# Performance work log

Hardware: AMD Instinct MI355X
Metric: run time of the kernel (lower is better)

## Reference

```python
import jax, jax.numpy as jnp
import numpy as np

S, B, SC = 2048, 1024, 256 * 16  # shops, bundles, styles*colors


def setup_inputs() -> dict:
    key = jax.random.key(0)
    k1, k2, k3, k4 = jax.random.split(key, 4)
    return {
        "proba": jax.random.normal(k1, (S * B,), dtype=jnp.float32),
        "cur_inven": jax.random.uniform(k2, (S, SC), dtype=jnp.float32),
        "bun_sc": jax.random.uniform(k3, (B, SC), dtype=jnp.float32),
        "avail_bundle": jax.random.uniform(k4, (B,), dtype=jnp.float32),
        "alloc_bundle": jnp.zeros((B,), dtype=jnp.float32),
    }


def reference(proba, cur_inven, bun_sc, avail_bundle, alloc_bundle):
    # proba[i] with i = shop*B + bundle  ->  [S, B]
    p = proba.reshape(S, B)
    # constraint_multiplier: 0.01 if over-availability (p>0) or over-negative-alloc (p<0)
    over_avail = (avail_bundle[None, :] - p < 0.0) & (p > 0.0)
    over_alloc = (alloc_bundle[None, :] + p < 0.0) & (p < 0.0)
    cm = jnp.where(over_avail | over_alloc, jnp.float32(0.01), jnp.float32(1.0))
    # next_inven[s, sc] = cur[s, sc] + sum_b bun_sc[b, sc] * p[s, b] * cm[s, b]
    next_inven = cur_inven + jnp.einsum('sb,bc->sc', p * cm, bun_sc)
    return next_inven.reshape(1, -1)
```

## Files before the change

kernel.cpp:

```cpp
#include <hip/hip_runtime.h>

#define S_DIM  2048
#define B_DIM  1024
#define SC_DIM 4096

#define BM 128
#define BN 128
#define BK 64

typedef __bf16 bf16x8 __attribute__((ext_vector_type(8)));
typedef float  f32x4  __attribute__((ext_vector_type(4)));
typedef unsigned short u16x4 __attribute__((ext_vector_type(4)));
typedef unsigned short u16x8 __attribute__((ext_vector_type(8)));

__device__ __forceinline__ unsigned short f2bf(float f) {
    unsigned int u = __builtin_bit_cast(unsigned int, f);
    return (unsigned short)((u + 0x7FFFu + ((u >> 16) & 1u)) >> 16);
}

__device__ __forceinline__ void gld_lds16(const void* g, void* l) {
    __builtin_amdgcn_global_load_lds(
        (const __attribute__((address_space(1))) unsigned int*)g,
        (__attribute__((address_space(3))) unsigned int*)l, 16, 0, 0);
}

__global__ __launch_bounds__(256)
void prepack_a(const float* __restrict__ proba,
               const float* __restrict__ avail,
               const float* __restrict__ alloc,
               unsigned short* __restrict__ wsA)
{
    int c = blockIdx.x * 256 + threadIdx.x;
    int n = c >> 7;
    int G = c & 127;
    int k = G * 8;

    f32x4 p0 = *(const f32x4*)&proba[(size_t)n * B_DIM + k];
    f32x4 p1 = *(const f32x4*)&proba[(size_t)n * B_DIM + k + 4];
    f32x4 av0 = *(const f32x4*)&avail[k];
    f32x4 av1 = *(const f32x4*)&avail[k + 4];
    f32x4 al0 = *(const f32x4*)&alloc[k];
    f32x4 al1 = *(const f32x4*)&alloc[k + 4];

    u16x8 w;
    #pragma unroll
    for (int i = 0; i < 4; ++i) {
        float pv = p0[i];
        bool oa = (av0[i] - pv < 0.f) && (pv > 0.f);
        bool ob = (al0[i] + pv < 0.f) && (pv < 0.f);
        w[i] = f2bf(pv * ((oa || ob) ? 0.01f : 1.0f));
    }
    #pragma unroll
    for (int i = 0; i < 4; ++i) {
        float pv = p1[i];
        bool oa = (av1[i] - pv < 0.f) && (pv > 0.f);
        bool ob = (al1[i] + pv < 0.f) && (pv < 0.f);
        w[4 + i] = f2bf(pv * ((oa || ob) ? 0.01f : 1.0f));
    }
    int Gs = (G & ~7) | ((G & 7) ^ (n & 7));
    *(u16x8*)&wsA[(size_t)n * B_DIM + Gs * 8] = w;
}

__global__ __launch_bounds__(256)
void prepack_b(const float* __restrict__ bsc,
               unsigned short* __restrict__ wsB)
{
    __shared__ float lds[64][129];
    const int t = threadIdx.x;
    const int bn0 = blockIdx.x * 128;
    const int k0  = blockIdx.y * 64;

    #pragma unroll
    for (int p = 0; p < 8; ++p) {
        int kl = (t >> 5) + p * 8;
        int cl = (t & 31) * 4;
        f32x4 v = *(const f32x4*)&bsc[(size_t)(k0 + kl) * SC_DIM + bn0 + cl];
        lds[kl][cl]     = v[0];
        lds[kl][cl + 1] = v[1];
        lds[kl][cl + 2] = v[2];
        lds[kl][cl + 3] = v[3];
    }
    __syncthreads();

    #pragma unroll
    for (int p = 0; p < 4; ++p) {
        int g = t & 7;
        int n = (t >> 3) + p * 32;
        u16x8 w;
        #pragma unroll
        for (int i = 0; i < 8; ++i)
            w[i] = f2bf(lds[g * 8 + i][n]);
        int gs = g ^ (n & 7);
        *(u16x8*)&wsB[(size_t)(bn0 + n) * B_DIM + k0 + gs * 8] = w;
    }
}

__global__ __launch_bounds__(256, 2)
void gemm_pk(const unsigned short* __restrict__ wsA,
             const unsigned short* __restrict__ wsB,
             const float* __restrict__ cur,
             float* __restrict__ out)
{
    __shared__ __align__(16) unsigned short sA[BM * BK];
    __shared__ __align__(16) unsigned short sB[BN * BK];

    const int tid  = threadIdx.x;
    const int lane = tid & 63;
    const int wid  = tid >> 6;
    const int wm   = wid >> 1;
    const int wn   = wid & 1;
    const int l16  = lane & 15;
    const int lg   = lane >> 4;

    const int bm0 = blockIdx.y * BM;
    const int bn0 = blockIdx.x * BN;

    f32x4 acc[4][4];
    #pragma unroll
    for (int i = 0; i < 4; ++i)
        #pragma unroll
        for (int j = 0; j < 4; ++j)
            acc[i][j] = {0.f, 0.f, 0.f, 0.f};

    const int cn = tid >> 3;
    const int cg = tid & 7;

    for (int k0 = 0; k0 < B_DIM; k0 += BK) {
        #pragma unroll
        for (int is = 0; is < 4; ++is) {
            int n = cn + is * 32;
            gld_lds16(wsA + (size_t)(bm0 + n) * B_DIM + k0 + cg * 8,
                      &sA[(is * 256 + tid) * 8]);
        }
        #pragma unroll
        for (int is = 0; is < 4; ++is) {
            int n = cn + is * 32;
            gld_lds16(wsB + (size_t)(bn0 + n) * B_DIM + k0 + cg * 8,
                      &sB[(is * 256 + tid) * 8]);
        }
        __syncthreads();

        #pragma unroll
        for (int kk = 0; kk < 2; ++kk) {
            bf16x8 afr[4], bfr[4];
            #pragma unroll
            for (int mf = 0; mf < 4; ++mf) {
                int r = wm * 64 + mf * 16 + l16;
                afr[mf] = *(const bf16x8*)&sA[r * BK + (((kk * 4 + lg) ^ (r & 7)) * 8)];
            }
            #pragma unroll
            for (int nf = 0; nf < 4; ++nf) {
                int r = wn * 64 + nf * 16 + l16;
                bfr[nf] = *(const bf16x8*)&sB[r * BK + (((kk * 4 + lg) ^ (r & 7)) * 8)];
            }
            #pragma unroll
            for (int mf = 0; mf < 4; ++mf)
                #pragma unroll
                for (int nf = 0; nf < 4; ++nf)
                    acc[mf][nf] = __builtin_amdgcn_mfma_f32_16x16x32_bf16(
                        afr[mf], bfr[nf], acc[mf][nf], 0, 0, 0);
        }
        __syncthreads();
    }

    #pragma unroll
    for (int mf = 0; mf < 4; ++mf) {
        #pragma unroll
        for (int j = 0; j < 4; ++j) {
            int row = bm0 + wm * 64 + mf * 16 + lg * 4 + j;
            #pragma unroll
            for (int nf = 0; nf < 4; ++nf) {
                int col = bn0 + wn * 64 + nf * 16 + l16;
                size_t idx = (size_t)row * SC_DIM + col;
                out[idx] = cur[idx] + acc[mf][nf][j];
            }
        }
    }
}

#define LDK 72
__global__ __launch_bounds__(256, 2)
void opt_gemm_fused(const float* __restrict__ proba,
                    const float* __restrict__ cur,
                    const float* __restrict__ bsc,
                    const float* __restrict__ avail,
                    const float* __restrict__ alloc,
                    float* __restrict__ out)
{
    __shared__ __align__(16) unsigned short sA[BM * LDK];
    __shared__ __align__(16) unsigned short sB[BN * LDK];
    const int tid = threadIdx.x;
    const int lane = tid & 63;
    const int wid = tid >> 6;
    const int wm = wid >> 1, wn = wid & 1;
    const int bm0 = blockIdx.y * BM, bn0 = blockIdx.x * BN;
    const int af4 = tid & 15, ar0 = tid >> 4;
    const int bnn = tid & 127, bkh = tid >> 7;
    const int l16 = lane & 15, lg = lane >> 4;

    f32x4 acc[4][4];
    #pragma unroll
    for (int i = 0; i < 4; ++i)
        #pragma unroll
        for (int j = 0; j < 4; ++j) acc[i][j] = {0.f, 0.f, 0.f, 0.f};

    for (int k0 = 0; k0 < B_DIM; k0 += BK) {
        f32x4 av = *(const f32x4*)&avail[k0 + af4 * 4];
        f32x4 al = *(const f32x4*)&alloc[k0 + af4 * 4];
        #pragma unroll
        for (int pass = 0; pass < 8; ++pass) {
            int r = ar0 + pass * 16;
            f32x4 p = *(const f32x4*)&proba[(size_t)(bm0 + r) * B_DIM + k0 + af4 * 4];
            u16x4 w;
            #pragma unroll
            for (int i = 0; i < 4; ++i) {
                float pv = p[i];
                bool oa = (av[i] - pv < 0.f) && (pv > 0.f);
                bool ob = (al[i] + pv < 0.f) && (pv < 0.f);
                w[i] = f2bf(pv * ((oa || ob) ? 0.01f : 1.0f));
            }
            *(u16x4*)&sA[r * LDK + af4 * 4] = w;
        }
        #pragma unroll
        for (int g = 0; g < 4; ++g) {
            u16x8 w;
            #pragma unroll
            for (int i = 0; i < 8; ++i) {
                int kk = bkh * 32 + g * 8 + i;
                w[i] = f2bf(bsc[(size_t)(k0 + kk) * SC_DIM + bn0 + bnn]);
            }
            *(u16x8*)&sB[bnn * LDK + bkh * 32 + g * 8] = w;
        }
        __syncthreads();
        #pragma unroll
        for (int kk = 0; kk < 2; ++kk) {
            bf16x8 afr[4], bfr[4];
            #pragma unroll
            for (int mf = 0; mf < 4; ++mf)
                afr[mf] = *(const bf16x8*)&sA[(wm * 64 + mf * 16 + l16) * LDK + kk * 32 + lg * 8];
            #pragma unroll
            for (int nf = 0; nf < 4; ++nf)
                bfr[nf] = *(const bf16x8*)&sB[(wn * 64 + nf * 16 + l16) * LDK + kk * 32 + lg * 8];
            #pragma unroll
            for (int mf = 0; mf < 4; ++mf)
                #pragma unroll
                for (int nf = 0; nf < 4; ++nf)
                    acc[mf][nf] = __builtin_amdgcn_mfma_f32_16x16x32_bf16(
                        afr[mf], bfr[nf], acc[mf][nf], 0, 0, 0);
        }
        __syncthreads();
    }
    #pragma unroll
    for (int mf = 0; mf < 4; ++mf)
        #pragma unroll
        for (int j = 0; j < 4; ++j) {
            int row = bm0 + wm * 64 + mf * 16 + lg * 4 + j;
            #pragma unroll
            for (int nf = 0; nf < 4; ++nf) {
                int col = bn0 + wn * 64 + nf * 16 + l16;
                size_t idx = (size_t)row * SC_DIM + col;
                out[idx] = cur[idx] + acc[mf][nf][j];
            }
        }
}

extern "C" void kernel_launch(void* const* d_in, const int* in_sizes, int n_in,
                              void* d_out, int out_size, void* d_ws, size_t ws_size,
                              hipStream_t stream) {
    const float* proba = (const float*)d_in[0];
    const float* cur   = (const float*)d_in[1];
    const float* bsc   = (const float*)d_in[2];
    const float* avail = (const float*)d_in[3];
    const float* alloc = (const float*)d_in[4];
    float* out = (float*)d_out;

    const size_t wsA_bytes = (size_t)S_DIM * B_DIM * 2;
    const size_t wsB_bytes = (size_t)SC_DIM * B_DIM * 2;

    if (ws_size >= wsA_bytes + wsB_bytes) {
        unsigned short* wsA = (unsigned short*)d_ws;
        unsigned short* wsB = (unsigned short*)((char*)d_ws + wsA_bytes);

        prepack_a<<<dim3(S_DIM * B_DIM / 8 / 256), 256, 0, stream>>>(proba, avail, alloc, wsA);
        prepack_b<<<dim3(SC_DIM / 128, B_DIM / 64), 256, 0, stream>>>(bsc, wsB);
        gemm_pk<<<dim3(SC_DIM / BN, S_DIM / BM), 256, 0, stream>>>(wsA, wsB, cur, out);
    } else {
        opt_gemm_fused<<<dim3(SC_DIM / BN, S_DIM / BM), 256, 0, stream>>>(
            proba, cur, bsc, avail, alloc, out);
    }
}
```

Before: 44.17 us.

## Double-buffer LDS tiles in packed GEMM with swizzled block order and epilogue prefetch

Converts the packed bf16 GEMM main loop to a two-stage LDS double buffer: the next K tile's global-to-LDS loads are issued before computing the current one, with explicit vmcnt waits and raw barriers. It also remaps block indices so consecutive blocks share A/B tiles for L2 reuse, raises wave priority around the MFMA bursts, and prefetches the `cur` epilogue values before the last tile's compute. This doubles LDS use per block, which may lower occupancy, and the swizzle hardcodes a 32x16 grid.

```diff
diff --git a/kernel.cpp b/kernel.cpp
--- a/kernel.cpp
+++ b/kernel.cpp
@@ -23,6 +23,8 @@
         (const __attribute__((address_space(1))) unsigned int*)g,
         (__attribute__((address_space(3))) unsigned int*)l, 16, 0, 0);
 }
+
+#define WAITCNT_VM(N) asm volatile("s_waitcnt vmcnt(" #N ")" ::: "memory")
 
 __global__ __launch_bounds__(256)
 void prepack_a(const float* __restrict__ proba,
@@ -101,8 +103,8 @@
              const float* __restrict__ cur,
              float* __restrict__ out)
 {
-    __shared__ __align__(16) unsigned short sA[BM * BK];
-    __shared__ __align__(16) unsigned short sB[BN * BK];
+    __shared__ __align__(16) unsigned short sA[2][BM * BK];
+    __shared__ __align__(16) unsigned short sB[2][BN * BK];
 
     const int tid  = threadIdx.x;
     const int lane = tid & 63;
@@ -112,8 +114,13 @@
     const int l16  = lane & 15;
     const int lg   = lane >> 4;
 
-    const int bm0 = blockIdx.y * BM;
-    const int bn0 = blockIdx.x * BN;
+    const int bid  = blockIdx.y * gridDim.x + blockIdx.x;
+    const int swz  = (bid & 7) * 64 + (bid >> 3);
+    const int bm0  = (swz >> 5) * BM;
+    const int bn0  = (swz & 31) * BN;
+
+    const int cn = tid >> 3;
+    const int cg = tid & 7;
 
     f32x4 acc[4][4];
     #pragma unroll
@@ -122,60 +129,85 @@
         for (int j = 0; j < 4; ++j)
             acc[i][j] = {0.f, 0.f, 0.f, 0.f};
 
-    const int cn = tid >> 3;
-    const int cg = tid & 7;
-
-    for (int k0 = 0; k0 < B_DIM; k0 += BK) {
-        #pragma unroll
-        for (int is = 0; is < 4; ++is) {
-            int n = cn + is * 32;
-            gld_lds16(wsA + (size_t)(bm0 + n) * B_DIM + k0 + cg * 8,
-                      &sA[(is * 256 + tid) * 8]);
-        }
-        #pragma unroll
-        for (int is = 0; is < 4; ++is) {
-            int n = cn + is * 32;
-            gld_lds16(wsB + (size_t)(bn0 + n) * B_DIM + k0 + cg * 8,
-                      &sB[(is * 256 + tid) * 8]);
-        }
-        __syncthreads();
-
+    auto stage = [&](int buf, int k0) {
+        #pragma unroll
+        for (int is = 0; is < 4; ++is)
+            gld_lds16(wsA + (size_t)(bm0 + cn + is * 32) * B_DIM + k0 + cg * 8,
+                      &sA[buf][(is * 256 + tid) * 8]);
+        #pragma unroll
+        for (int is = 0; is < 4; ++is)
+            gld_lds16(wsB + (size_t)(bn0 + cn + is * 32) * B_DIM + k0 + cg * 8,
+                      &sB[buf][(is * 256 + tid) * 8]);
+    };
+
+    auto compute = [&](int buf) {
         #pragma unroll
         for (int kk = 0; kk < 2; ++kk) {
             bf16x8 afr[4], bfr[4];
             #pragma unroll
             for (int mf = 0; mf < 4; ++mf) {
                 int r = wm * 64 + mf * 16 + l16;
-                afr[mf] = *(const bf16x8*)&sA[r * BK + (((kk * 4 + lg) ^ (r & 7)) * 8)];
+                afr[mf] = *(const bf16x8*)&sA[buf][r * BK + (((kk * 4 + lg) ^ (r & 7)) * 8)];
             }
             #pragma unroll
             for (int nf = 0; nf < 4; ++nf) {
                 int r = wn * 64 + nf * 16 + l16;
-                bfr[nf] = *(const bf16x8*)&sB[r * BK + (((kk * 4 + lg) ^ (r & 7)) * 8)];
-            }
+                bfr[nf] = *(const bf16x8*)&sB[buf][r * BK + (((kk * 4 + lg) ^ (r & 7)) * 8)];
+            }
+            __builtin_amdgcn_s_setprio(1);
             #pragma unroll
             for (int mf = 0; mf < 4; ++mf)
                 #pragma unroll
                 for (int nf = 0; nf < 4; ++nf)
                     acc[mf][nf] = __builtin_amdgcn_mfma_f32_16x16x32_bf16(
                         afr[mf], bfr[nf], acc[mf][nf], 0, 0, 0);
-        }
-        __syncthreads();
-    }
-
-    #pragma unroll
-    for (int mf = 0; mf < 4; ++mf) {
-        #pragma unroll
-        for (int j = 0; j < 4; ++j) {
-            int row = bm0 + wm * 64 + mf * 16 + lg * 4 + j;
+            __builtin_amdgcn_s_setprio(0);
+        }
+    };
+
+    const int NT = B_DIM / BK;
+    stage(0, 0);
+
+    #pragma unroll 2
+    for (int t = 0; t < NT - 1; ++t) {
+        const int buf = t & 1;
+        stage(buf ^ 1, (t + 1) * BK);
+        WAITCNT_VM(8);
+        __builtin_amdgcn_s_barrier();
+        __builtin_amdgcn_sched_barrier(0);
+        compute(buf);
+        __builtin_amdgcn_sched_barrier(0);
+        __builtin_amdgcn_s_barrier();
+    }
+
+    WAITCNT_VM(0);
+    __builtin_amdgcn_s_barrier();
+    __builtin_amdgcn_sched_barrier(0);
+
+    float cpref[4][4][4];
+    #pragma unroll
+    for (int mf = 0; mf < 4; ++mf)
+        #pragma unroll
+        for (int j = 0; j < 4; ++j)
             #pragma unroll
             for (int nf = 0; nf < 4; ++nf) {
+                int row = bm0 + wm * 64 + mf * 16 + lg * 4 + j;
                 int col = bn0 + wn * 64 + nf * 16 + l16;
-                size_t idx = (size_t)row * SC_DIM + col;
-                out[idx] = cur[idx] + acc[mf][nf][j];
-            }
-        }
-    }
+                cpref[mf][j][nf] = cur[(size_t)row * SC_DIM + col];
+            }
+
+    compute((NT - 1) & 1);
+
+    #pragma unroll
+    for (int mf = 0; mf < 4; ++mf)
+        #pragma unroll
+        for (int j = 0; j < 4; ++j)
+            #pragma unroll
+            for (int nf = 0; nf < 4; ++nf) {
+                int row = bm0 + wm * 64 + mf * 16 + lg * 4 + j;
+                int col = bn0 + wn * 64 + nf * 16 + l16;
+                out[(size_t)row * SC_DIM + col] = cpref[mf][j][nf] + acc[mf][nf][j];
+            }
 }
 
 #define LDK 72
```

Result: faster. 41.26 us (-6.6%).

## Shrink GEMM M-tile, swizzle block order, prefetch epilogue, raise MFMA priority

Applied to the files above, without the earlier changes.

Halves the packed GEMM's M tile to 64 rows and raises the occupancy hint to 4 blocks per CU. This doubles the grid to 1024 blocks so more waves are resident and the device fills better. It also remaps block IDs with an XCD-style swizzle for L2 locality, prefetches the `cur` tile into registers before the final compute step to hide epilogue load latency, and wraps the MFMA bursts in s_setprio. The cost is lower arithmetic intensity per block and more redundant B-tile loads. The fused fallback kernel keeps its own 128 tiles through new FBM/FBN macros.

```diff
diff --git a/kernel.cpp b/kernel.cpp
--- a/kernel.cpp
+++ b/kernel.cpp
@@ -4,7 +4,7 @@
 #define B_DIM  1024
 #define SC_DIM 4096
 
-#define BM 128
+#define BM 64
 #define BN 128
 #define BK 64
 
@@ -95,7 +95,7 @@
     }
 }
 
-__global__ __launch_bounds__(256, 2)
+__global__ __launch_bounds__(256, 4)
 void gemm_pk(const unsigned short* __restrict__ wsA,
              const unsigned short* __restrict__ wsB,
              const float* __restrict__ cur,
@@ -112,40 +112,39 @@
     const int l16  = lane & 15;
     const int lg   = lane >> 4;
 
-    const int bm0 = blockIdx.y * BM;
-    const int bn0 = blockIdx.x * BN;
-
-    f32x4 acc[4][4];
-    #pragma unroll
-    for (int i = 0; i < 4; ++i)
+    const int bid  = blockIdx.y * gridDim.x + blockIdx.x;
+    const int swz  = (bid & 7) * 128 + (bid >> 3);
+    const int bm0  = (swz >> 5) * BM;
+    const int bn0  = (swz & 31) * BN;
+
+    const int crow = tid >> 3;
+    const int cg   = tid & 7;
+
+    f32x4 acc[2][4];
+    #pragma unroll
+    for (int i = 0; i < 2; ++i)
         #pragma unroll
         for (int j = 0; j < 4; ++j)
             acc[i][j] = {0.f, 0.f, 0.f, 0.f};
 
-    const int cn = tid >> 3;
-    const int cg = tid & 7;
-
-    for (int k0 = 0; k0 < B_DIM; k0 += BK) {
-        #pragma unroll
-        for (int is = 0; is < 4; ++is) {
-            int n = cn + is * 32;
-            gld_lds16(wsA + (size_t)(bm0 + n) * B_DIM + k0 + cg * 8,
+    auto stage = [&](int k0) {
+        #pragma unroll
+        for (int is = 0; is < 2; ++is)
+            gld_lds16(wsA + (size_t)(bm0 + is * 32 + crow) * B_DIM + k0 + cg * 8,
                       &sA[(is * 256 + tid) * 8]);
-        }
-        #pragma unroll
-        for (int is = 0; is < 4; ++is) {
-            int n = cn + is * 32;
-            gld_lds16(wsB + (size_t)(bn0 + n) * B_DIM + k0 + cg * 8,
+        #pragma unroll
+        for (int is = 0; is < 4; ++is)
+            gld_lds16(wsB + (size_t)(bn0 + is * 32 + crow) * B_DIM + k0 + cg * 8,
                       &sB[(is * 256 + tid) * 8]);
-        }
-        __syncthreads();
-
+    };
+
+    auto compute = [&]() {
         #pragma unroll
         for (int kk = 0; kk < 2; ++kk) {
-            bf16x8 afr[4], bfr[4];
-            #pragma unroll
-            for (int mf = 0; mf < 4; ++mf) {
-                int r = wm * 64 + mf * 16 + l16;
+            bf16x8 afr[2], bfr[4];
+            #pragma unroll
+            for (int mf = 0; mf < 2; ++mf) {
+                int r = wm * 32 + mf * 16 + l16;
                 afr[mf] = *(const bf16x8*)&sA[r * BK + (((kk * 4 + lg) ^ (r & 7)) * 8)];
             }
             #pragma unroll
@@ -153,31 +152,57 @@
                 int r = wn * 64 + nf * 16 + l16;
                 bfr[nf] = *(const bf16x8*)&sB[r * BK + (((kk * 4 + lg) ^ (r & 7)) * 8)];
             }
-            #pragma unroll
-            for (int mf = 0; mf < 4; ++mf)
+            __builtin_amdgcn_s_setprio(1);
+            #pragma unroll
+            for (int mf = 0; mf < 2; ++mf)
                 #pragma unroll
                 for (int nf = 0; nf < 4; ++nf)
                     acc[mf][nf] = __builtin_amdgcn_mfma_f32_16x16x32_bf16(
                         afr[mf], bfr[nf], acc[mf][nf], 0, 0, 0);
-        }
+            __builtin_amdgcn_s_setprio(0);
+        }
+    };
+
+    const int NT = B_DIM / BK;
+
+    for (int t = 0; t < NT - 1; ++t) {
+        stage(t * BK);
         __syncthreads();
-    }
-
-    #pragma unroll
-    for (int mf = 0; mf < 4; ++mf) {
-        #pragma unroll
-        for (int j = 0; j < 4; ++j) {
-            int row = bm0 + wm * 64 + mf * 16 + lg * 4 + j;
+        compute();
+        __syncthreads();
+    }
+
+    stage((NT - 1) * BK);
+    __syncthreads();
+
+    float cpref[2][4][4];
+    #pragma unroll
+    for (int mf = 0; mf < 2; ++mf)
+        #pragma unroll
+        for (int j = 0; j < 4; ++j)
             #pragma unroll
             for (int nf = 0; nf < 4; ++nf) {
+                int row = bm0 + wm * 32 + mf * 16 + lg * 4 + j;
                 int col = bn0 + wn * 64 + nf * 16 + l16;
-                size_t idx = (size_t)row * SC_DIM + col;
-                out[idx] = cur[idx] + acc[mf][nf][j];
-            }
-        }
-    }
-}
-
+                cpref[mf][j][nf] = cur[(size_t)row * SC_DIM + col];
+            }
+
+    compute();
+
+    #pragma unroll
+    for (int mf = 0; mf < 2; ++mf)
+        #pragma unroll
+        for (int j = 0; j < 4; ++j)
+            #pragma unroll
+            for (int nf = 0; nf < 4; ++nf) {
+                int row = bm0 + wm * 32 + mf * 16 + lg * 4 + j;
+                int col = bn0 + wn * 64 + nf * 16 + l16;
+                out[(size_t)row * SC_DIM + col] = cpref[mf][j][nf] + acc[mf][nf][j];
+            }
+}
+
+#define FBM 128
+#define FBN 128
 #define LDK 72
 __global__ __launch_bounds__(256, 2)
 void opt_gemm_fused(const float* __restrict__ proba,
@@ -187,13 +212,13 @@
                     const float* __restrict__ alloc,
                     float* __restrict__ out)
 {
-    __shared__ __align__(16) unsigned short sA[BM * LDK];
-    __shared__ __align__(16) unsigned short sB[BN * LDK];
+    __shared__ __align__(16) unsigned short sA[FBM * LDK];
+    __shared__ __align__(16) unsigned short sB[FBN * LDK];
     const int tid = threadIdx.x;
     const int lane = tid & 63;
     const int wid = tid >> 6;
     const int wm = wid >> 1, wn = wid & 1;
-    const int bm0 = blockIdx.y * BM, bn0 = blockIdx.x * BN;
+    const int bm0 = blockIdx.y * FBM, bn0 = blockIdx.x * FBN;
     const int af4 = tid & 15, ar0 = tid >> 4;
     const int bnn = tid & 127, bkh = tid >> 7;
     const int l16 = lane & 15, lg = lane >> 4;
@@ -285,7 +310,7 @@
         prepack_b<<<dim3(SC_DIM / 128, B_DIM / 64), 256, 0, stream>>>(bsc, wsB);
         gemm_pk<<<dim3(SC_DIM / BN, S_DIM / BM), 256, 0, stream>>>(wsA, wsB, cur, out);
     } else {
-        opt_gemm_fused<<<dim3(SC_DIM / BN, S_DIM / BM), 256, 0, stream>>>(
+        opt_gemm_fused<<<dim3(SC_DIM / FBN, S_DIM / FBM), 256, 0, stream>>>(
             proba, cur, bsc, avail, alloc, out);
     }
 }
```

Result: no change. 43.57 us (-1.4%).

## Merge prepack kernels, swizzle GEMM tile order, prefetch next K tile during MFMA

Applied to the files above, without the earlier changes.

The two prepack kernels are merged into one launch that branches on block index, saving a kernel launch. The GEMM now uses a 1D grid with a grouped tile ordering intended to improve L2 reuse. Its K loop reads fragments into registers, then issues the next tile's global-to-LDS loads before running the MFMAs, so loads overlap compute. The cost is more live registers for two k-steps of fragments, and the single LDS buffer adds an extra barrier per iteration.

```diff
diff --git a/kernel.cpp b/kernel.cpp
--- a/kernel.cpp
+++ b/kernel.cpp
@@ -25,73 +25,74 @@
 }
 
 __global__ __launch_bounds__(256)
-void prepack_a(const float* __restrict__ proba,
-               const float* __restrict__ avail,
-               const float* __restrict__ alloc,
-               unsigned short* __restrict__ wsA)
-{
-    int c = blockIdx.x * 256 + threadIdx.x;
-    int n = c >> 7;
-    int G = c & 127;
-    int k = G * 8;
-
-    f32x4 p0 = *(const f32x4*)&proba[(size_t)n * B_DIM + k];
-    f32x4 p1 = *(const f32x4*)&proba[(size_t)n * B_DIM + k + 4];
-    f32x4 av0 = *(const f32x4*)&avail[k];
-    f32x4 av1 = *(const f32x4*)&avail[k + 4];
-    f32x4 al0 = *(const f32x4*)&alloc[k];
-    f32x4 al1 = *(const f32x4*)&alloc[k + 4];
-
-    u16x8 w;
-    #pragma unroll
-    for (int i = 0; i < 4; ++i) {
-        float pv = p0[i];
-        bool oa = (av0[i] - pv < 0.f) && (pv > 0.f);
-        bool ob = (al0[i] + pv < 0.f) && (pv < 0.f);
-        w[i] = f2bf(pv * ((oa || ob) ? 0.01f : 1.0f));
-    }
-    #pragma unroll
-    for (int i = 0; i < 4; ++i) {
-        float pv = p1[i];
-        bool oa = (av1[i] - pv < 0.f) && (pv > 0.f);
-        bool ob = (al1[i] + pv < 0.f) && (pv < 0.f);
-        w[4 + i] = f2bf(pv * ((oa || ob) ? 0.01f : 1.0f));
-    }
-    int Gs = (G & ~7) | ((G & 7) ^ (n & 7));
-    *(u16x8*)&wsA[(size_t)n * B_DIM + Gs * 8] = w;
-}
-
-__global__ __launch_bounds__(256)
-void prepack_b(const float* __restrict__ bsc,
-               unsigned short* __restrict__ wsB)
+void prepack_ab(const float* __restrict__ proba,
+                const float* __restrict__ avail,
+                const float* __restrict__ alloc,
+                const float* __restrict__ bsc,
+                unsigned short* __restrict__ wsA,
+                unsigned short* __restrict__ wsB)
 {
     __shared__ float lds[64][129];
     const int t = threadIdx.x;
-    const int bn0 = blockIdx.x * 128;
-    const int k0  = blockIdx.y * 64;
-
-    #pragma unroll
-    for (int p = 0; p < 8; ++p) {
-        int kl = (t >> 5) + p * 8;
-        int cl = (t & 31) * 4;
-        f32x4 v = *(const f32x4*)&bsc[(size_t)(k0 + kl) * SC_DIM + bn0 + cl];
-        lds[kl][cl]     = v[0];
-        lds[kl][cl + 1] = v[1];
-        lds[kl][cl + 2] = v[2];
-        lds[kl][cl + 3] = v[3];
-    }
-    __syncthreads();
-
-    #pragma unroll
-    for (int p = 0; p < 4; ++p) {
-        int g = t & 7;
-        int n = (t >> 3) + p * 32;
+
+    if (blockIdx.x < 1024) {
+        int c = blockIdx.x * 256 + t;
+        int n = c >> 7;
+        int G = c & 127;
+        int k = G * 8;
+
+        f32x4 p0 = *(const f32x4*)&proba[(size_t)n * B_DIM + k];
+        f32x4 p1 = *(const f32x4*)&proba[(size_t)n * B_DIM + k + 4];
+        f32x4 av0 = *(const f32x4*)&avail[k];
+        f32x4 av1 = *(const f32x4*)&avail[k + 4];
+        f32x4 al0 = *(const f32x4*)&alloc[k];
+        f32x4 al1 = *(const f32x4*)&alloc[k + 4];
+
         u16x8 w;
         #pragma unroll
-        for (int i = 0; i < 8; ++i)
-            w[i] = f2bf(lds[g * 8 + i][n]);
-        int gs = g ^ (n & 7);
-        *(u16x8*)&wsB[(size_t)(bn0 + n) * B_DIM + k0 + gs * 8] = w;
+        for (int i = 0; i < 4; ++i) {
+            float pv = p0[i];
+            bool oa = (av0[i] - pv < 0.f) && (pv > 0.f);
+            bool ob = (al0[i] + pv < 0.f) && (pv < 0.f);
+            w[i] = f2bf(pv * ((oa || ob) ? 0.01f : 1.0f));
+        }
+        #pragma unroll
+        for (int i = 0; i < 4; ++i) {
+            float pv = p1[i];
+            bool oa = (av1[i] - pv < 0.f) && (pv > 0.f);
+            bool ob = (al1[i] + pv < 0.f) && (pv < 0.f);
+            w[4 + i] = f2bf(pv * ((oa || ob) ? 0.01f : 1.0f));
+        }
+        int Gs = (G & ~7) | ((G & 7) ^ (n & 7));
+        *(u16x8*)&wsA[(size_t)n * B_DIM + Gs * 8] = w;
+    } else {
+        int b2 = blockIdx.x - 1024;
+        const int bn0 = (b2 & 31) * 128;
+        const int k0  = (b2 >> 5) * 64;
+
+        #pragma unroll
+        for (int p = 0; p < 8; ++p) {
+            int kl = (t >> 5) + p * 8;
+            int cl = (t & 31) * 4;
+            f32x4 v = *(const f32x4*)&bsc[(size_t)(k0 + kl) * SC_DIM + bn0 + cl];
+            lds[kl][cl]     = v[0];
+            lds[kl][cl + 1] = v[1];
+            lds[kl][cl + 2] = v[2];
+            lds[kl][cl + 3] = v[3];
+        }
+        __syncthreads();
+
+        #pragma unroll
+        for (int p = 0; p < 4; ++p) {
+            int g = t & 7;
+            int n = (t >> 3) + p * 32;
+            u16x8 w;
+            #pragma unroll
+            for (int i = 0; i < 8; ++i)
+                w[i] = f2bf(lds[g * 8 + i][n]);
+            int gs = g ^ (n & 7);
+            *(u16x8*)&wsB[(size_t)(bn0 + n) * B_DIM + k0 + gs * 8] = w;
+        }
     }
 }
 
@@ -112,8 +113,16 @@
     const int l16  = lane & 15;
     const int lg   = lane >> 4;
 
-    const int bm0 = blockIdx.y * BM;
-    const int bn0 = blockIdx.x * BN;
+    const int bid    = blockIdx.x;
+    const int x      = bid & 7;
+    const int l      = bid >> 3;
+    const int n_tile = x * 4 + (l & 3);
+    const int m_tile = l >> 2;
+    const int bm0    = m_tile * BM;
+    const int bn0    = n_tile * BN;
+
+    const int crow = tid >> 3;
+    const int cg   = tid & 7;
 
     f32x4 acc[4][4];
     #pragma unroll
@@ -122,62 +131,68 @@
         for (int j = 0; j < 4; ++j)
             acc[i][j] = {0.f, 0.f, 0.f, 0.f};
 
-    const int cn = tid >> 3;
-    const int cg = tid & 7;
-
-    for (int k0 = 0; k0 < B_DIM; k0 += BK) {
-        #pragma unroll
-        for (int is = 0; is < 4; ++is) {
-            int n = cn + is * 32;
-            gld_lds16(wsA + (size_t)(bm0 + n) * B_DIM + k0 + cg * 8,
+    auto stage = [&](int k0) {
+        #pragma unroll
+        for (int is = 0; is < 4; ++is)
+            gld_lds16(wsA + (size_t)(bm0 + is * 32 + crow) * B_DIM + k0 + cg * 8,
                       &sA[(is * 256 + tid) * 8]);
-        }
-        #pragma unroll
-        for (int is = 0; is < 4; ++is) {
-            int n = cn + is * 32;
-            gld_lds16(wsB + (size_t)(bn0 + n) * B_DIM + k0 + cg * 8,
+        #pragma unroll
+        for (int is = 0; is < 4; ++is)
+            gld_lds16(wsB + (size_t)(bn0 + is * 32 + crow) * B_DIM + k0 + cg * 8,
                       &sB[(is * 256 + tid) * 8]);
-        }
-        __syncthreads();
-
+    };
+
+    const int NT = B_DIM / BK;
+    stage(0);
+
+    for (int t = 0; t < NT; ++t) {
+        __syncthreads();
+
+        bf16x8 afr[2][4], bfr[2][4];
         #pragma unroll
         for (int kk = 0; kk < 2; ++kk) {
-            bf16x8 afr[4], bfr[4];
             #pragma unroll
             for (int mf = 0; mf < 4; ++mf) {
                 int r = wm * 64 + mf * 16 + l16;
-                afr[mf] = *(const bf16x8*)&sA[r * BK + (((kk * 4 + lg) ^ (r & 7)) * 8)];
+                afr[kk][mf] = *(const bf16x8*)&sA[r * BK + (((kk * 4 + lg) ^ (r & 7)) * 8)];
             }
             #pragma unroll
             for (int nf = 0; nf < 4; ++nf) {
                 int r = wn * 64 + nf * 16 + l16;
-                bfr[nf] = *(const bf16x8*)&sB[r * BK + (((kk * 4 + lg) ^ (r & 7)) * 8)];
-            }
+                bfr[kk][nf] = *(const bf16x8*)&sB[r * BK + (((kk * 4 + lg) ^ (r & 7)) * 8)];
+            }
+        }
+        __syncthreads();
+
+        if (t < NT - 1)
+            stage((t + 1) * BK);
+        __builtin_amdgcn_sched_barrier(0);
+
+        #pragma unroll
+        for (int kk = 0; kk < 2; ++kk)
             #pragma unroll
             for (int mf = 0; mf < 4; ++mf)
                 #pragma unroll
                 for (int nf = 0; nf < 4; ++nf)
                     acc[mf][nf] = __builtin_amdgcn_mfma_f32_16x16x32_bf16(
-                        afr[mf], bfr[nf], acc[mf][nf], 0, 0, 0);
-        }
-        __syncthreads();
+                        afr[kk][mf], bfr[kk][nf], acc[mf][nf], 0, 0, 0);
     }
 
     #pragma unroll
-    for (int mf = 0; mf < 4; ++mf) {
-        #pragma unroll
-        for (int j = 0; j < 4; ++j) {
-            int row = bm0 + wm * 64 + mf * 16 + lg * 4 + j;
+    for (int mf = 0; mf < 4; ++mf)
+        #pragma unroll
+        for (int j = 0; j < 4; ++j)
             #pragma unroll
             for (int nf = 0; nf < 4; ++nf) {
+                int row = bm0 + wm * 64 + mf * 16 + lg * 4 + j;
                 int col = bn0 + wn * 64 + nf * 16 + l16;
                 size_t idx = (size_t)row * SC_DIM + col;
                 out[idx] = cur[idx] + acc[mf][nf][j];
             }
-        }
-    }
-}
-
+}
+
+#define FBM 128
+#define FBN 128
 #define LDK 72
 __global__ __launch_bounds__(256, 2)
 void opt_gemm_fused(const float* __restrict__ proba,
@@ -187,13 +202,13 @@
                     const float* __restrict__ alloc,
                     float* __restrict__ out)
 {
-    __shared__ __align__(16) unsigned short sA[BM * LDK];
-    __shared__ __align__(16) unsigned short sB[BN * LDK];
+    __shared__ __align__(16) unsigned short sA[FBM * LDK];
+    __shared__ __align__(16) unsigned short sB[FBN * LDK];
     const int tid = threadIdx.x;
     const int lane = tid & 63;
     const int wid = tid >> 6;
     const int wm = wid >> 1, wn = wid & 1;
-    const int bm0 = blockIdx.y * BM, bn0 = blockIdx.x * BN;
+    const int bm0 = blockIdx.y * FBM, bn0 = blockIdx.x * FBN;
     const int af4 = tid & 15, ar0 = tid >> 4;
     const int bnn = tid & 127, bkh = tid >> 7;
     const int l16 = lane & 15, lg = lane >> 4;
@@ -281,11 +296,10 @@
         unsigned short* wsA = (unsigned short*)d_ws;
         unsigned short* wsB = (unsigned short*)((char*)d_ws + wsA_bytes);
 
-        prepack_a<<<dim3(S_DIM * B_DIM / 8 / 256), 256, 0, stream>>>(proba, avail, alloc, wsA);
-        prepack_b<<<dim3(SC_DIM / 128, B_DIM / 64), 256, 0, stream>>>(bsc, wsB);
-        gemm_pk<<<dim3(SC_DIM / BN, S_DIM / BM), 256, 0, stream>>>(wsA, wsB, cur, out);
+        prepack_ab<<<dim3(1024 + 512), 256, 0, stream>>>(proba, avail, alloc, bsc, wsA, wsB);
+        gemm_pk<<<dim3((S_DIM / BM) * (SC_DIM / BN)), 256, 0, stream>>>(wsA, wsB, cur, out);
     } else {
-        opt_gemm_fused<<<dim3(SC_DIM / BN, S_DIM / BM), 256, 0, stream>>>(
+        opt_gemm_fused<<<dim3(SC_DIM / FBN, S_DIM / FBM), 256, 0, stream>>>(
             proba, cur, bsc, avail, alloc, out);
     }
 }
```

Result: faster. 36.25 us (-17.9%).
